# Performance work log

Measured on AMD Instinct MI355X. Metric: run time of the kernel, lower is better.

Reference implementation:

```python
import jax, jax.numpy as jnp
import numpy as np

HIDDEN = 256
NUM_STEPS = 3
N_NODES = 200000
N_GRAPHS = 512


def setup_inputs() -> dict:
    key = jax.random.key(0)
    ks = jax.random.split(key, 8)
    h = HIDDEN
    x = jax.random.normal(ks[0], (N_NODES, h), dtype=jnp.float32)
    batch = jnp.sort(jax.random.randint(ks[1], (N_NODES,), 0, N_GRAPHS)).astype(jnp.int64)
    s_ih = 1.0 / np.sqrt(2 * h)
    s_hh = 1.0 / np.sqrt(h)
    # LSTM (input 2h -> hidden h), PyTorch gate order i,f,g,o
    W_ih = jax.random.uniform(ks[2], (4 * h, 2 * h), jnp.float32, -s_ih, s_ih)
    W_hh = jax.random.uniform(ks[3], (4 * h, h), jnp.float32, -s_hh, s_hh)
    b_ih = jax.random.uniform(ks[4], (4 * h,), jnp.float32, -s_hh, s_hh)
    b_hh = jax.random.uniform(ks[5], (4 * h,), jnp.float32, -s_hh, s_hh)
    # out_proj: Linear(2h -> h)
    s_o = 1.0 / np.sqrt(2 * h)
    W_out = jax.random.uniform(ks[6], (h, 2 * h), jnp.float32, -s_o, s_o)
    b_out = jax.random.uniform(ks[7], (h,), jnp.float32, -s_o, s_o)
    return {"x": x, "batch": batch, "W_ih": W_ih, "W_hh": W_hh,
            "b_ih": b_ih, "b_hh": b_hh, "W_out": W_out, "b_out": b_out,
            "n_graphs": N_GRAPHS}


def _set2set(x, batch, W_ih, W_hh, b_ih, b_hh, n_graphs):
    h = x.shape[1]
    hs = jnp.zeros((n_graphs, h), x.dtype)
    cs = jnp.zeros((n_graphs, h), x.dtype)
    q_star = jnp.zeros((n_graphs, 2 * h), x.dtype)
    for _ in range(NUM_STEPS):
        # LSTM step (PyTorch gate order: i, f, g, o)
        gates = q_star @ W_ih.T + hs @ W_hh.T + (b_ih + b_hh)  # [B, 4h]
        i_g, f_g, g_g, o_g = jnp.split(gates, 4, axis=-1)
        cs = jax.nn.sigmoid(f_g) * cs + jax.nn.sigmoid(i_g) * jnp.tanh(g_g)
        hs = jax.nn.sigmoid(o_g) * jnp.tanh(cs)
        q = hs  # [B, h]
        # attention logits per node
        e = jnp.sum(x * q[batch], axis=-1)  # [N]
        # segment softmax over nodes of each graph
        m = jax.ops.segment_max(e, batch, num_segments=n_graphs)
        a = jnp.exp(e - m[batch])
        denom = jax.ops.segment_sum(a, batch, num_segments=n_graphs)
        a = a / denom[batch]
        # weighted readout
        r = jax.ops.segment_sum(a[:, None] * x, batch, num_segments=n_graphs)  # [B, h]
        q_star = jnp.concatenate([q, r], axis=-1)  # [B, 2h]
    return q_star


def reference(x, batch, W_ih, W_hh, b_ih, b_hh, W_out, b_out, n_graphs):
    q_star = _set2set(x, batch.astype(jnp.int32), W_ih, W_hh, b_ih, b_hh, n_graphs)
    return q_star @ W_out.T + b_out
```

## Files before the change

kernel.cpp:

```cpp
#include <hip/hip_runtime.h>
#include <hip/hip_bf16.h>

#define HID 256
#define NG 512

__device__ __forceinline__ float sigmoidf_(float v) { return 1.f / (1.f + __expf(-v)); }

__global__ __launch_bounds__(256) void prep_kernel(
    const float* __restrict__ W_ih, const float* __restrict__ W_hh,
    const float* __restrict__ b_ih, const float* __restrict__ b_hh,
    float* __restrict__ Wcat, float* __restrict__ bcat)
{
    int idx = blockIdx.x * 256 + threadIdx.x;
    if (idx < 1024 * 512) {
        int k = idx & 511;
        float v = W_ih[idx];
        if (k < 256) v += W_hh[(idx >> 9) * 256 + k];
        Wcat[idx] = v;
    }
    if (idx < 1024) bcat[idx] = b_ih[idx] + b_hh[idx];
}

__global__ __launch_bounds__(256) void find_starts(
    const int* __restrict__ batch, int n, int* __restrict__ starts)
{
    int g = blockIdx.x * 256 + threadIdx.x;
    if (g > NG) return;
    if (g == NG) { starts[NG] = n; return; }
    int lo = 0, hi = n;
    while (lo < hi) {
        int mid = (lo + hi) >> 1;
        if (batch[mid] < g) lo = mid + 1; else hi = mid;
    }
    starts[g] = lo;
}

__global__ __launch_bounds__(256) void attn_kernel(
    const float* __restrict__ x, const int* __restrict__ starts,
    const float* __restrict__ gp0, const float* __restrict__ gp1,
    const float* __restrict__ bcat, float* __restrict__ cs,
    float* __restrict__ qs, int step0)
{
    __shared__ __align__(16) float ql[HID];
    __shared__ __align__(16) float red[4][HID];
    __shared__ float mw[4], lw[4];

    const int g = blockIdx.x;
    const int tid = threadIdx.x;

    float ig, fg, gg, og, cp;
    if (step0) {
        ig = bcat[tid]; fg = bcat[256 + tid]; gg = bcat[512 + tid]; og = bcat[768 + tid];
        cp = 0.f;
    } else {
        const float* a0 = gp0 + (size_t)g * 1024;
        const float* a1 = gp1 + (size_t)g * 1024;
        ig = a0[tid]       + a1[tid]       + bcat[tid];
        fg = a0[256 + tid] + a1[256 + tid] + bcat[256 + tid];
        gg = a0[512 + tid] + a1[512 + tid] + bcat[512 + tid];
        og = a0[768 + tid] + a1[768 + tid] + bcat[768 + tid];
        cp = cs[g * HID + tid];
    }
    float cn = sigmoidf_(fg) * cp + sigmoidf_(ig) * tanhf(gg);
    float h  = sigmoidf_(og) * tanhf(cn);
    cs[g * HID + tid] = cn;
    qs[(size_t)g * 512 + tid] = h;
    ql[tid] = h;

    const int s0 = starts[g];
    const int nn = starts[g + 1] - s0;
    if (nn <= 0) { qs[(size_t)g * 512 + HID + tid] = 0.f; return; }
    __syncthreads();

    const int w = tid >> 6, lane = tid & 63;
    const int j = lane >> 3;
    const int s = lane & 7;

    float4 qf[8];
    #pragma unroll
    for (int k = 0; k < 8; ++k) qf[k] = *(const float4*)&ql[k * 32 + s * 4];

    const int nch = (nn + 7) >> 3;
    const int last = s0 + nn - 1;
    const float NEG = -3.402823466e38f;

    float m_run = NEG, l_run = 0.f;
    float4 racc[8] = {};
    float4 xc[8], xn[8];

    int c = w;
    if (c < nch) {
        int node = s0 + c * 8 + j; if (node > last) node = last;
        const float* bp = x + (size_t)node * HID + s * 4;
        #pragma unroll
        for (int k = 0; k < 8; ++k) xc[k] = *(const float4*)(bp + k * 32);
    }
    for (; c < nch; c += 4) {
        if (c + 4 < nch) {
            int node = s0 + (c + 4) * 8 + j; if (node > last) node = last;
            const float* bp = x + (size_t)node * HID + s * 4;
            #pragma unroll
            for (int k = 0; k < 8; ++k) xn[k] = *(const float4*)(bp + k * 32);
        }
        const bool valid = (c * 8 + j) < nn;

        float e = 0.f;
        #pragma unroll
        for (int k = 0; k < 8; ++k)
            e += xc[k].x * qf[k].x + xc[k].y * qf[k].y + xc[k].z * qf[k].z + xc[k].w * qf[k].w;
        e += __shfl_xor(e, 1); e += __shfl_xor(e, 2); e += __shfl_xor(e, 4);
        e = valid ? e : NEG;

        float mc = e;
        mc = fmaxf(mc, __shfl_xor(mc, 8));
        mc = fmaxf(mc, __shfl_xor(mc, 16));
        mc = fmaxf(mc, __shfl_xor(mc, 32));
        float m_new = fmaxf(m_run, mc);
        float alpha = __expf(m_run - m_new);
        float p = valid ? __expf(e - m_new) : 0.f;
        float ps = p;
        ps += __shfl_xor(ps, 8); ps += __shfl_xor(ps, 16); ps += __shfl_xor(ps, 32);
        l_run = l_run * alpha + ps;
        m_run = m_new;
        #pragma unroll
        for (int k = 0; k < 8; ++k) {
            racc[k].x = racc[k].x * alpha + p * xc[k].x;
            racc[k].y = racc[k].y * alpha + p * xc[k].y;
            racc[k].z = racc[k].z * alpha + p * xc[k].z;
            racc[k].w = racc[k].w * alpha + p * xc[k].w;
        }
        #pragma unroll
        for (int k = 0; k < 8; ++k) xc[k] = xn[k];
    }

    #pragma unroll
    for (int k = 0; k < 8; ++k) {
        racc[k].x += __shfl_xor(racc[k].x, 8);
        racc[k].y += __shfl_xor(racc[k].y, 8);
        racc[k].z += __shfl_xor(racc[k].z, 8);
        racc[k].w += __shfl_xor(racc[k].w, 8);
        racc[k].x += __shfl_xor(racc[k].x, 16);
        racc[k].y += __shfl_xor(racc[k].y, 16);
        racc[k].z += __shfl_xor(racc[k].z, 16);
        racc[k].w += __shfl_xor(racc[k].w, 16);
        racc[k].x += __shfl_xor(racc[k].x, 32);
        racc[k].y += __shfl_xor(racc[k].y, 32);
        racc[k].z += __shfl_xor(racc[k].z, 32);
        racc[k].w += __shfl_xor(racc[k].w, 32);
    }
    if (j == 0) {
        #pragma unroll
        for (int k = 0; k < 8; ++k) *(float4*)&red[w][k * 32 + s * 4] = racc[k];
        if (s == 0) { mw[w] = m_run; lw[w] = l_run; }
    }
    __syncthreads();

    float M = fmaxf(fmaxf(mw[0], mw[1]), fmaxf(mw[2], mw[3]));
    float f0 = __expf(mw[0] - M), f1 = __expf(mw[1] - M);
    float f2 = __expf(mw[2] - M), f3 = __expf(mw[3] - M);
    float L = lw[0] * f0 + lw[1] * f1 + lw[2] * f2 + lw[3] * f3;
    float r = red[0][tid] * f0 + red[1][tid] * f1 + red[2][tid] * f2 + red[3][tid] * f3;
    qs[(size_t)g * 512 + HID + tid] = r / L;
}

__global__ __launch_bounds__(256) void gemm_splitk(
    const float* __restrict__ A, int lda,
    const float* __restrict__ B, int ldb,
    float* __restrict__ Cp, int ldc, int KS, size_t slice_stride)
{
    __shared__ float As[16][76];
    __shared__ float Bs[16][76];
    const int tid = threadIdx.x;
    const int tx = tid & 15, ty = tid >> 4;
    const int m0 = blockIdx.y * 64, n0 = blockIdx.x * 64;
    const int kb = blockIdx.z * KS;
    const int r = tid >> 2, kc = (tid & 3) << 2;
    float acc[4][4] = {};

    const float* Ap = &A[(size_t)(m0 + r) * lda + kb + kc];
    const float* Bp = &B[(size_t)(n0 + r) * ldb + kb + kc];
    float4 av = *(const float4*)Ap;
    float4 bv = *(const float4*)Bp;

    for (int k0 = 0; k0 < KS; k0 += 16) {
        As[kc + 0][r] = av.x; As[kc + 1][r] = av.y; As[kc + 2][r] = av.z; As[kc + 3][r] = av.w;
        Bs[kc + 0][r] = bv.x; Bs[kc + 1][r] = bv.y; Bs[kc + 2][r] = bv.z; Bs[kc + 3][r] = bv.w;
        __syncthreads();
        if (k0 + 16 < KS) {
            av = *(const float4*)(Ap + k0 + 16);
            bv = *(const float4*)(Bp + k0 + 16);
        }
        #pragma unroll
        for (int kk = 0; kk < 16; ++kk) {
            float4 a = *(const float4*)&As[kk][ty << 2];
            float4 b = *(const float4*)&Bs[kk][tx << 2];
            acc[0][0] += a.x * b.x; acc[0][1] += a.x * b.y; acc[0][2] += a.x * b.z; acc[0][3] += a.x * b.w;
            acc[1][0] += a.y * b.x; acc[1][1] += a.y * b.y; acc[1][2] += a.y * b.z; acc[1][3] += a.y * b.w;
            acc[2][0] += a.z * b.x; acc[2][1] += a.z * b.y; acc[2][2] += a.z * b.z; acc[2][3] += a.z * b.w;
            acc[3][0] += a.w * b.x; acc[3][1] += a.w * b.y; acc[3][2] += a.w * b.z; acc[3][3] += a.w * b.w;
        }
        __syncthreads();
    }
    float* out = Cp + blockIdx.z * slice_stride;
    #pragma unroll
    for (int i = 0; i < 4; ++i) {
        float4 o = make_float4(acc[i][0], acc[i][1], acc[i][2], acc[i][3]);
        *(float4*)&out[(size_t)(m0 + ty * 4 + i) * ldc + n0 + (tx << 2)] = o;
    }
}

__global__ __launch_bounds__(256) void finalize_out(
    const float* __restrict__ op, const float* __restrict__ b_out,
    float* __restrict__ out)
{
    int i = blockIdx.x * 256 + threadIdx.x;
    if (i < 512 * 256) {
        float v = op[i] + op[131072 + i] + op[262144 + i] + op[393216 + i] + b_out[i & 255];
        out[i] = v;
    }
}

extern "C" void kernel_launch(void* const* d_in, const int* in_sizes, int n_in,
                              void* d_out, int out_size, void* d_ws, size_t ws_size,
                              hipStream_t stream)
{
    const float* x     = (const float*)d_in[0];
    const int*   batch = (const int*)d_in[1];
    const float* W_ih  = (const float*)d_in[2];
    const float* W_hh  = (const float*)d_in[3];
    const float* b_ih  = (const float*)d_in[4];
    const float* b_hh  = (const float*)d_in[5];
    const float* W_out = (const float*)d_in[6];
    const float* b_out = (const float*)d_in[7];
    float* out = (float*)d_out;
    const int n = in_sizes[1];
    (void)n_in; (void)out_size; (void)ws_size;

    char* ws = (char*)d_ws;
    float* qs      = (float*)(ws);
    float* cs      = (float*)(ws + 0x100000);
    float* gates_p = (float*)(ws + 0x180000);
    float* Wcat    = (float*)(ws + 0x580000);
    float* bcat    = (float*)(ws + 0x780000);
    int*   starts  = (int*)  (ws + 0x781000);
    float* out_p   = (float*)(ws + 0x790000);

    prep_kernel<<<2048, 256, 0, stream>>>(W_ih, W_hh, b_ih, b_hh, Wcat, bcat);
    find_starts<<<3, 256, 0, stream>>>(batch, n, starts);

    for (int step = 0; step < 3; ++step) {
        if (step > 0) {
            gemm_splitk<<<dim3(16, 8, 2), 256, 0, stream>>>(
                qs, 512, Wcat, 512, gates_p, 1024, 256, (size_t)512 * 1024);
        }
        attn_kernel<<<NG, 256, 0, stream>>>(
            x, starts, gates_p, gates_p + (size_t)512 * 1024, bcat, cs, qs, step == 0);
    }
    gemm_splitk<<<dim3(4, 8, 4), 256, 0, stream>>>(
        qs, 512, W_out, 512, out_p, 256, 128, (size_t)512 * 256);
    finalize_out<<<512, 256, 0, stream>>>(out_p, b_out, out);
}
```

Baseline: 413.5 us.

## Fuse all Set2Set stages into one cooperative persistent kernel with grid syncs

```diff
diff --git a/kernel.cpp b/kernel.cpp
--- a/kernel.cpp
+++ b/kernel.cpp
@@ -1,222 +1,244 @@
 #include <hip/hip_runtime.h>
 #include <hip/hip_bf16.h>
+#include <hip/hip_cooperative_groups.h>
+
+namespace cg = cooperative_groups;
 
 #define HID 256
 #define NG 512
+#define NBLK 256
 
 __device__ __forceinline__ float sigmoidf_(float v) { return 1.f / (1.f + __expf(-v)); }
 
-__global__ __launch_bounds__(256) void prep_kernel(
-    const float* __restrict__ W_ih, const float* __restrict__ W_hh,
-    const float* __restrict__ b_ih, const float* __restrict__ b_hh,
-    float* __restrict__ Wcat, float* __restrict__ bcat)
-{
-    int idx = blockIdx.x * 256 + threadIdx.x;
-    if (idx < 1024 * 512) {
-        int k = idx & 511;
-        float v = W_ih[idx];
-        if (k < 256) v += W_hh[(idx >> 9) * 256 + k];
-        Wcat[idx] = v;
-    }
-    if (idx < 1024) bcat[idx] = b_ih[idx] + b_hh[idx];
-}
-
-__global__ __launch_bounds__(256) void find_starts(
-    const int* __restrict__ batch, int n, int* __restrict__ starts)
-{
-    int g = blockIdx.x * 256 + threadIdx.x;
-    if (g > NG) return;
-    if (g == NG) { starts[NG] = n; return; }
-    int lo = 0, hi = n;
-    while (lo < hi) {
-        int mid = (lo + hi) >> 1;
-        if (batch[mid] < g) lo = mid + 1; else hi = mid;
-    }
-    starts[g] = lo;
-}
-
-__global__ __launch_bounds__(256) void attn_kernel(
+struct SM {
+    float As[16][76];
+    float Bs[16][76];
+    float ql[HID];
+    float red[4][HID];
+    float mw[4], lw[4];
+};
+
+__device__ __forceinline__ void gemm_tile(
+    const float* __restrict__ A, int lda, const float* __restrict__ B, int ldb,
+    float* __restrict__ C, int ldc, int m0, int n0, int kb, int KS,
+    SM& sm, int tid)
+{
+    const int tx = tid & 15, ty = tid >> 4;
+    const int r = tid >> 2, kc = (tid & 3) << 2;
+    float acc[4][4] = {};
+    const float* Ap = &A[(size_t)(m0 + r) * lda + kb + kc];
+    const float* Bp = &B[(size_t)(n0 + r) * ldb + kb + kc];
+    float4 av = *(const float4*)Ap;
+    float4 bv = *(const float4*)Bp;
+    for (int k0 = 0; k0 < KS; k0 += 16) {
+        sm.As[kc + 0][r] = av.x; sm.As[kc + 1][r] = av.y;
+        sm.As[kc + 2][r] = av.z; sm.As[kc + 3][r] = av.w;
+        sm.Bs[kc + 0][r] = bv.x; sm.Bs[kc + 1][r] = bv.y;
+        sm.Bs[kc + 2][r] = bv.z; sm.Bs[kc + 3][r] = bv.w;
+        __syncthreads();
+        if (k0 + 16 < KS) {
+            av = *(const float4*)(Ap + k0 + 16);
+            bv = *(const float4*)(Bp + k0 + 16);
+        }
+        #pragma unroll
+        for (int kk = 0; kk < 16; ++kk) {
+            float4 a  = *(const float4*)&sm.As[kk][ty << 2];
+            float4 b4 = *(const float4*)&sm.Bs[kk][tx << 2];
+            acc[0][0] += a.x * b4.x; acc[0][1] += a.x * b4.y; acc[0][2] += a.x * b4.z; acc[0][3] += a.x * b4.w;
+            acc[1][0] += a.y * b4.x; acc[1][1] += a.y * b4.y; acc[1][2] += a.y * b4.z; acc[1][3] += a.y * b4.w;
+            acc[2][0] += a.z * b4.x; acc[2][1] += a.z * b4.y; acc[2][2] += a.z * b4.z; acc[2][3] += a.z * b4.w;
+            acc[3][0] += a.w * b4.x; acc[3][1] += a.w * b4.y; acc[3][2] += a.w * b4.z; acc[3][3] += a.w * b4.w;
+        }
+        __syncthreads();
+    }
+    #pragma unroll
+    for (int i = 0; i < 4; ++i) {
+        float4 o = make_float4(acc[i][0], acc[i][1], acc[i][2], acc[i][3]);
+        *(float4*)&C[(size_t)(m0 + ty * 4 + i) * ldc + n0 + (tx << 2)] = o;
+    }
+}
+
+__device__ void attn_graph(
     const float* __restrict__ x, const int* __restrict__ starts,
-    const float* __restrict__ gp0, const float* __restrict__ gp1,
-    const float* __restrict__ bcat, float* __restrict__ cs,
-    float* __restrict__ qs, int step0)
-{
-    __shared__ __align__(16) float ql[HID];
-    __shared__ __align__(16) float red[4][HID];
-    __shared__ float mw[4], lw[4];
-
-    const int g = blockIdx.x;
-    const int tid = threadIdx.x;
-
-    float ig, fg, gg, og, cp;
+    const float* __restrict__ gp, const float* __restrict__ bcat,
+    float* __restrict__ qs, float& cstate,
+    int g, int tid, int step0, SM& sm)
+{
+    float ig, fg, gg, og;
     if (step0) {
         ig = bcat[tid]; fg = bcat[256 + tid]; gg = bcat[512 + tid]; og = bcat[768 + tid];
-        cp = 0.f;
     } else {
-        const float* a0 = gp0 + (size_t)g * 1024;
-        const float* a1 = gp1 + (size_t)g * 1024;
+        const float* a0 = gp + (size_t)g * 1024;
+        const float* a1 = a0 + (size_t)512 * 1024;
         ig = a0[tid]       + a1[tid]       + bcat[tid];
         fg = a0[256 + tid] + a1[256 + tid] + bcat[256 + tid];
         gg = a0[512 + tid] + a1[512 + tid] + bcat[512 + tid];
         og = a0[768 + tid] + a1[768 + tid] + bcat[768 + tid];
-        cp = cs[g * HID + tid];
-    }
+    }
+    float cp = step0 ? 0.f : cstate;
     float cn = sigmoidf_(fg) * cp + sigmoidf_(ig) * tanhf(gg);
     float h  = sigmoidf_(og) * tanhf(cn);
-    cs[g * HID + tid] = cn;
+    cstate = cn;
     qs[(size_t)g * 512 + tid] = h;
-    ql[tid] = h;
+    sm.ql[tid] = h;
 
     const int s0 = starts[g];
     const int nn = starts[g + 1] - s0;
-    if (nn <= 0) { qs[(size_t)g * 512 + HID + tid] = 0.f; return; }
     __syncthreads();
 
-    const int w = tid >> 6, lane = tid & 63;
-    const int j = lane >> 3;
-    const int s = lane & 7;
-
-    float4 qf[8];
-    #pragma unroll
-    for (int k = 0; k < 8; ++k) qf[k] = *(const float4*)&ql[k * 32 + s * 4];
-
-    const int nch = (nn + 7) >> 3;
-    const int last = s0 + nn - 1;
-    const float NEG = -3.402823466e38f;
-
-    float m_run = NEG, l_run = 0.f;
-    float4 racc[8] = {};
-    float4 xc[8], xn[8];
-
-    int c = w;
-    if (c < nch) {
-        int node = s0 + c * 8 + j; if (node > last) node = last;
-        const float* bp = x + (size_t)node * HID + s * 4;
+    float rout = 0.f;
+    if (nn > 0) {
+        const int w = tid >> 6, lane = tid & 63;
+        const int j = lane >> 3;
+        const int s = lane & 7;
+
+        float4 qf[8];
         #pragma unroll
-        for (int k = 0; k < 8; ++k) xc[k] = *(const float4*)(bp + k * 32);
-    }
-    for (; c < nch; c += 4) {
-        if (c + 4 < nch) {
-            int node = s0 + (c + 4) * 8 + j; if (node > last) node = last;
+        for (int k = 0; k < 8; ++k) qf[k] = *(const float4*)&sm.ql[k * 32 + s * 4];
+
+        const int nch = (nn + 7) >> 3;
+        const int last = s0 + nn - 1;
+        const float NEG = -3.402823466e38f;
+
+        float m_run = NEG, l_run = 0.f;
+        float4 racc[8] = {};
+        float4 xc[8], xn[8];
+
+        int c = w;
+        if (c < nch) {
+            int node = s0 + c * 8 + j; if (node > last) node = last;
             const float* bp = x + (size_t)node * HID + s * 4;
             #pragma unroll
-            for (int k = 0; k < 8; ++k) xn[k] = *(const float4*)(bp + k * 32);
-        }
-        const bool valid = (c * 8 + j) < nn;
-
-        float e = 0.f;
-        #pragma unroll
-        for (int k = 0; k < 8; ++k)
-            e += xc[k].x * qf[k].x + xc[k].y * qf[k].y + xc[k].z * qf[k].z + xc[k].w * qf[k].w;
-        e += __shfl_xor(e, 1); e += __shfl_xor(e, 2); e += __shfl_xor(e, 4);
-        e = valid ? e : NEG;
-
-        float mc = e;
-        mc = fmaxf(mc, __shfl_xor(mc, 8));
-        mc = fmaxf(mc, __shfl_xor(mc, 16));
-        mc = fmaxf(mc, __shfl_xor(mc, 32));
-        float m_new = fmaxf(m_run, mc);
-        float alpha = __expf(m_run - m_new);
-        float p = valid ? __expf(e - m_new) : 0.f;
-        float ps = p;
-        ps += __shfl_xor(ps, 8); ps += __shfl_xor(ps, 16); ps += __shfl_xor(ps, 32);
-        l_run = l_run * alpha + ps;
-        m_run = m_new;
+            for (int k = 0; k < 8; ++k) xc[k] = *(const float4*)(bp + k * 32);
+        }
+        for (; c < nch; c += 4) {
+            if (c + 4 < nch) {
+                int node = s0 + (c + 4) * 8 + j; if (node > last) node = last;
+                const float* bp = x + (size_t)node * HID + s * 4;
+                #pragma unroll
+                for (int k = 0; k < 8; ++k) xn[k] = *(const float4*)(bp + k * 32);
+            }
+            const bool valid = (c * 8 + j) < nn;
+
+            float e = 0.f;
+            #pragma unroll
+            for (int k = 0; k < 8; ++k)
+                e += xc[k].x * qf[k].x + xc[k].y * qf[k].y + xc[k].z * qf[k].z + xc[k].w * qf[k].w;
+            e += __shfl_xor(e, 1); e += __shfl_xor(e, 2); e += __shfl_xor(e, 4);
+            e = valid ? e : NEG;
+
+            float mc = e;
+            mc = fmaxf(mc, __shfl_xor(mc, 8));
+            mc = fmaxf(mc, __shfl_xor(mc, 16));
+            mc = fmaxf(mc, __shfl_xor(mc, 32));
+            float m_new = fmaxf(m_run, mc);
+            float alpha = __expf(m_run - m_new);
+            float p = valid ? __expf(e - m_new) : 0.f;
+            float ps = p;
+            ps += __shfl_xor(ps, 8); ps += __shfl_xor(ps, 16); ps += __shfl_xor(ps, 32);
+            l_run = l_run * alpha + ps;
+            m_run = m_new;
+            #pragma unroll
+            for (int k = 0; k < 8; ++k) {
+                racc[k].x = racc[k].x * alpha + p * xc[k].x;
+                racc[k].y = racc[k].y * alpha + p * xc[k].y;
+                racc[k].z = racc[k].z * alpha + p * xc[k].z;
+                racc[k].w = racc[k].w * alpha + p * xc[k].w;
+            }
+            #pragma unroll
+            for (int k = 0; k < 8; ++k) xc[k] = xn[k];
+        }
+
         #pragma unroll
         for (int k = 0; k < 8; ++k) {
-            racc[k].x = racc[k].x * alpha + p * xc[k].x;
-            racc[k].y = racc[k].y * alpha + p * xc[k].y;
-            racc[k].z = racc[k].z * alpha + p * xc[k].z;
-            racc[k].w = racc[k].w * alpha + p * xc[k].w;
-        }
-        #pragma unroll
-        for (int k = 0; k < 8; ++k) xc[k] = xn[k];
-    }
+            racc[k].x += __shfl_xor(racc[k].x, 8);  racc[k].y += __shfl_xor(racc[k].y, 8);
+            racc[k].z += __shfl_xor(racc[k].z, 8);  racc[k].w += __shfl_xor(racc[k].w, 8);
+            racc[k].x += __shfl_xor(racc[k].x, 16); racc[k].y += __shfl_xor(racc[k].y, 16);
+            racc[k].z += __shfl_xor(racc[k].z, 16); racc[k].w += __shfl_xor(racc[k].w, 16);
+            racc[k].x += __shfl_xor(racc[k].x, 32); racc[k].y += __shfl_xor(racc[k].y, 32);
+            racc[k].z += __shfl_xor(racc[k].z, 32); racc[k].w += __shfl_xor(racc[k].w, 32);
+        }
+        if (j == 0) {
+            #pragma unroll
+            for (int k = 0; k < 8; ++k) *(float4*)&sm.red[w][k * 32 + s * 4] = racc[k];
+            if (s == 0) { sm.mw[w] = m_run; sm.lw[w] = l_run; }
+        }
+        __syncthreads();
+
+        float M = fmaxf(fmaxf(sm.mw[0], sm.mw[1]), fmaxf(sm.mw[2], sm.mw[3]));
+        float f0 = __expf(sm.mw[0] - M), f1 = __expf(sm.mw[1] - M);
+        float f2 = __expf(sm.mw[2] - M), f3 = __expf(sm.mw[3] - M);
+        float L = sm.lw[0] * f0 + sm.lw[1] * f1 + sm.lw[2] * f2 + sm.lw[3] * f3;
+        float r = sm.red[0][tid] * f0 + sm.red[1][tid] * f1
+                + sm.red[2][tid] * f2 + sm.red[3][tid] * f3;
+        rout = r / L;
+    }
+    qs[(size_t)g * 512 + HID + tid] = rout;
+    __syncthreads();
+}
+
+__global__ __launch_bounds__(256) void fused_kernel(
+    const float* __restrict__ x, const int* __restrict__ batch,
+    const float* __restrict__ W_ih, const float* __restrict__ W_hh,
+    const float* __restrict__ b_ih, const float* __restrict__ b_hh,
+    const float* __restrict__ W_out, const float* __restrict__ b_out,
+    float* __restrict__ out, int n, char* __restrict__ ws)
+{
+    __shared__ SM sm;
+    float* qs     = (float*)(ws);
+    float* gp     = (float*)(ws + 0x100000);
+    float* Wcat   = (float*)(ws + 0x500000);
+    float* bcat   = (float*)(ws + 0x700000);
+    int*   starts = (int*)  (ws + 0x701000);
+    float* op     = (float*)(ws + 0x710000);
+
+    cg::grid_group grid = cg::this_grid();
+    const int b = blockIdx.x, tid = threadIdx.x;
+    const int gtid = b * 256 + tid;
 
     #pragma unroll
-    for (int k = 0; k < 8; ++k) {
-        racc[k].x += __shfl_xor(racc[k].x, 8);
-        racc[k].y += __shfl_xor(racc[k].y, 8);
-        racc[k].z += __shfl_xor(racc[k].z, 8);
-        racc[k].w += __shfl_xor(racc[k].w, 8);
-        racc[k].x += __shfl_xor(racc[k].x, 16);
-        racc[k].y += __shfl_xor(racc[k].y, 16);
-        racc[k].z += __shfl_xor(racc[k].z, 16);
-        racc[k].w += __shfl_xor(racc[k].w, 16);
-        racc[k].x += __shfl_xor(racc[k].x, 32);
-        racc[k].y += __shfl_xor(racc[k].y, 32);
-        racc[k].z += __shfl_xor(racc[k].z, 32);
-        racc[k].w += __shfl_xor(racc[k].w, 32);
-    }
-    if (j == 0) {
-        #pragma unroll
-        for (int k = 0; k < 8; ++k) *(float4*)&red[w][k * 32 + s * 4] = racc[k];
-        if (s == 0) { mw[w] = m_run; lw[w] = l_run; }
-    }
-    __syncthreads();
-
-    float M = fmaxf(fmaxf(mw[0], mw[1]), fmaxf(mw[2], mw[3]));
-    float f0 = __expf(mw[0] - M), f1 = __expf(mw[1] - M);
-    float f2 = __expf(mw[2] - M), f3 = __expf(mw[3] - M);
-    float L = lw[0] * f0 + lw[1] * f1 + lw[2] * f2 + lw[3] * f3;
-    float r = red[0][tid] * f0 + red[1][tid] * f1 + red[2][tid] * f2 + red[3][tid] * f3;
-    qs[(size_t)g * 512 + HID + tid] = r / L;
-}
-
-__global__ __launch_bounds__(256) void gemm_splitk(
-    const float* __restrict__ A, int lda,
-    const float* __restrict__ B, int ldb,
-    float* __restrict__ Cp, int ldc, int KS, size_t slice_stride)
-{
-    __shared__ float As[16][76];
-    __shared__ float Bs[16][76];
-    const int tid = threadIdx.x;
-    const int tx = tid & 15, ty = tid >> 4;
-    const int m0 = blockIdx.y * 64, n0 = blockIdx.x * 64;
-    const int kb = blockIdx.z * KS;
-    const int r = tid >> 2, kc = (tid & 3) << 2;
-    float acc[4][4] = {};
-
-    const float* Ap = &A[(size_t)(m0 + r) * lda + kb + kc];
-    const float* Bp = &B[(size_t)(n0 + r) * ldb + kb + kc];
-    float4 av = *(const float4*)Ap;
-    float4 bv = *(const float4*)Bp;
-
-    for (int k0 = 0; k0 < KS; k0 += 16) {
-        As[kc + 0][r] = av.x; As[kc + 1][r] = av.y; As[kc + 2][r] = av.z; As[kc + 3][r] = av.w;
-        Bs[kc + 0][r] = bv.x; Bs[kc + 1][r] = bv.y; Bs[kc + 2][r] = bv.z; Bs[kc + 3][r] = bv.w;
-        __syncthreads();
-        if (k0 + 16 < KS) {
-            av = *(const float4*)(Ap + k0 + 16);
-            bv = *(const float4*)(Bp + k0 + 16);
-        }
-        #pragma unroll
-        for (int kk = 0; kk < 16; ++kk) {
-            float4 a = *(const float4*)&As[kk][ty << 2];
-            float4 b = *(const float4*)&Bs[kk][tx << 2];
-            acc[0][0] += a.x * b.x; acc[0][1] += a.x * b.y; acc[0][2] += a.x * b.z; acc[0][3] += a.x * b.w;
-            acc[1][0] += a.y * b.x; acc[1][1] += a.y * b.y; acc[1][2] += a.y * b.z; acc[1][3] += a.y * b.w;
-            acc[2][0] += a.z * b.x; acc[2][1] += a.z * b.y; acc[2][2] += a.z * b.z; acc[2][3] += a.z * b.w;
-            acc[3][0] += a.w * b.x; acc[3][1] += a.w * b.y; acc[3][2] += a.w * b.z; acc[3][3] += a.w * b.w;
-        }
-        __syncthreads();
-    }
-    float* out = Cp + blockIdx.z * slice_stride;
-    #pragma unroll
-    for (int i = 0; i < 4; ++i) {
-        float4 o = make_float4(acc[i][0], acc[i][1], acc[i][2], acc[i][3]);
-        *(float4*)&out[(size_t)(m0 + ty * 4 + i) * ldc + n0 + (tx << 2)] = o;
-    }
-}
-
-__global__ __launch_bounds__(256) void finalize_out(
-    const float* __restrict__ op, const float* __restrict__ b_out,
-    float* __restrict__ out)
-{
-    int i = blockIdx.x * 256 + threadIdx.x;
-    if (i < 512 * 256) {
-        float v = op[i] + op[131072 + i] + op[262144 + i] + op[393216 + i] + b_out[i & 255];
-        out[i] = v;
+    for (int t = 0; t < 2; ++t) {
+        int o = (gtid * 2 + t) * 4;
+        int k = o & 511, row = o >> 9;
+        float4 v = *(const float4*)&W_ih[o];
+        if (k < 256) {
+            float4 u = *(const float4*)&W_hh[row * 256 + k];
+            v.x += u.x; v.y += u.y; v.z += u.z; v.w += u.w;
+        }
+        *(float4*)&Wcat[o] = v;
+    }
+    if (gtid < 1024) bcat[gtid] = b_ih[gtid] + b_hh[gtid];
+    for (int i = gtid; i < n; i += NBLK * 256) {
+        int b1 = batch[i];
+        int b0 = (i == 0) ? -1 : batch[i - 1];
+        for (int g2 = b0 + 1; g2 <= b1; ++g2) starts[g2] = i;
+        if (i == n - 1) for (int g2 = b1 + 1; g2 <= NG; ++g2) starts[g2] = n;
+    }
+    grid.sync();
+
+    float c0 = 0.f, c1 = 0.f;
+    for (int step = 0; step < 3; ++step) {
+        if (step > 0) {
+            int bz = b >> 7, by = (b >> 4) & 7, bx = b & 15;
+            gemm_tile(qs, 512, Wcat, 512, gp + (size_t)bz * 512 * 1024, 1024,
+                      by * 64, bx * 64, bz * 256, 256, sm, tid);
+            grid.sync();
+        }
+        attn_graph(x, starts, gp, bcat, qs, c0, 2 * b,     tid, step == 0, sm);
+        attn_graph(x, starts, gp, bcat, qs, c1, 2 * b + 1, tid, step == 0, sm);
+        grid.sync();
+    }
+
+    if (b < 128) {
+        int bz = b >> 5, by = (b >> 2) & 7, bx = b & 3;
+        gemm_tile(qs, 512, W_out, 512, op + (size_t)bz * 512 * 256, 256,
+                  by * 64, bx * 64, bz * 128, 128, sm, tid);
+    }
+    grid.sync();
+    {
+        int i0 = gtid, i1 = gtid + 65536;
+        out[i0] = op[i0] + op[131072 + i0] + op[262144 + i0] + op[393216 + i0] + b_out[i0 & 255];
+        out[i1] = op[i1] + op[131072 + i1] + op[262144 + i1] + op[393216 + i1] + b_out[i1 & 255];
     }
 }
 
@@ -233,30 +255,13 @@
     const float* W_out = (const float*)d_in[6];
     const float* b_out = (const float*)d_in[7];
     float* out = (float*)d_out;
-    const int n = in_sizes[1];
+    int n = in_sizes[1];
+    char* ws = (char*)d_ws;
     (void)n_in; (void)out_size; (void)ws_size;
 
-    char* ws = (char*)d_ws;
-    float* qs      = (float*)(ws);
-    float* cs      = (float*)(ws + 0x100000);
-    float* gates_p = (float*)(ws + 0x180000);
-    float* Wcat    = (float*)(ws + 0x580000);
-    float* bcat    = (float*)(ws + 0x780000);
-    int*   starts  = (int*)  (ws + 0x781000);
-    float* out_p   = (float*)(ws + 0x790000);
-
-    prep_kernel<<<2048, 256, 0, stream>>>(W_ih, W_hh, b_ih, b_hh, Wcat, bcat);
-    find_starts<<<3, 256, 0, stream>>>(batch, n, starts);
-
-    for (int step = 0; step < 3; ++step) {
-        if (step > 0) {
-            gemm_splitk<<<dim3(16, 8, 2), 256, 0, stream>>>(
-                qs, 512, Wcat, 512, gates_p, 1024, 256, (size_t)512 * 1024);
-        }
-        attn_kernel<<<NG, 256, 0, stream>>>(
-            x, starts, gates_p, gates_p + (size_t)512 * 1024, bcat, cs, qs, step == 0);
-    }
-    gemm_splitk<<<dim3(4, 8, 4), 256, 0, stream>>>(
-        qs, 512, W_out, 512, out_p, 256, 128, (size_t)512 * 256);
-    finalize_out<<<512, 256, 0, stream>>>(out_p, b_out, out);
-}
+    void* args[] = { (void*)&x, (void*)&batch, (void*)&W_ih, (void*)&W_hh,
+                     (void*)&b_ih, (void*)&b_hh, (void*)&W_out, (void*)&b_out,
+                     (void*)&out, (void*)&n, (void*)&ws };
+    hipLaunchCooperativeKernel((const void*)fused_kernel, dim3(NBLK), dim3(256),
+                               args, 0, stream);
+}
```

Result: slower. 627.8 us (+51.8%).

## Deepen x prefetch, keep per-lane online softmax, fuse prep and starts kernels

Applied to the files above, without the earlier changes.

```diff
diff --git a/kernel.cpp b/kernel.cpp
--- a/kernel.cpp
+++ b/kernel.cpp
@@ -9,37 +9,39 @@
 __global__ __launch_bounds__(256) void prep_kernel(
     const float* __restrict__ W_ih, const float* __restrict__ W_hh,
     const float* __restrict__ b_ih, const float* __restrict__ b_hh,
-    float* __restrict__ Wcat, float* __restrict__ bcat)
-{
-    int idx = blockIdx.x * 256 + threadIdx.x;
-    if (idx < 1024 * 512) {
-        int k = idx & 511;
-        float v = W_ih[idx];
-        if (k < 256) v += W_hh[(idx >> 9) * 256 + k];
-        Wcat[idx] = v;
-    }
-    if (idx < 1024) bcat[idx] = b_ih[idx] + b_hh[idx];
-}
-
-__global__ __launch_bounds__(256) void find_starts(
-    const int* __restrict__ batch, int n, int* __restrict__ starts)
-{
-    int g = blockIdx.x * 256 + threadIdx.x;
-    if (g > NG) return;
-    if (g == NG) { starts[NG] = n; return; }
-    int lo = 0, hi = n;
-    while (lo < hi) {
-        int mid = (lo + hi) >> 1;
-        if (batch[mid] < g) lo = mid + 1; else hi = mid;
-    }
-    starts[g] = lo;
-}
-
-__global__ __launch_bounds__(256) void attn_kernel(
+    const int* __restrict__ batch, int n,
+    float* __restrict__ Wcat, float* __restrict__ bcat, int* __restrict__ starts)
+{
+    int b = blockIdx.x, tid = threadIdx.x;
+    if (b < 512) {
+        int o = (b * 256 + tid) * 4;
+        int k = o & 511, row = o >> 9;
+        float4 v = *(const float4*)&W_ih[o];
+        if (k < 256) {
+            float4 u = *(const float4*)&W_hh[row * 256 + k];
+            v.x += u.x; v.y += u.y; v.z += u.z; v.w += u.w;
+        }
+        *(float4*)&Wcat[o] = v;
+    } else if (b < 516) {
+        int i = (b - 512) * 256 + tid;
+        bcat[i] = b_ih[i] + b_hh[i];
+    } else {
+        int g = (b - 516) * 256 + tid;
+        if (g > NG) return;
+        if (g == NG) { starts[NG] = n; return; }
+        int lo = 0, hi = n;
+        while (lo < hi) {
+            int mid = (lo + hi) >> 1;
+            if (batch[mid] < g) lo = mid + 1; else hi = mid;
+        }
+        starts[g] = lo;
+    }
+}
+
+__global__ __launch_bounds__(256, 2) void attn_kernel(
     const float* __restrict__ x, const int* __restrict__ starts,
-    const float* __restrict__ gp0, const float* __restrict__ gp1,
-    const float* __restrict__ bcat, float* __restrict__ cs,
-    float* __restrict__ qs, int step0)
+    const float* __restrict__ gp, const float* __restrict__ bcat,
+    float* __restrict__ cs, float* __restrict__ qs, int step0)
 {
     __shared__ __align__(16) float ql[HID];
     __shared__ __align__(16) float red[4][HID];
@@ -48,19 +50,18 @@
     const int g = blockIdx.x;
     const int tid = threadIdx.x;
 
-    float ig, fg, gg, og, cp;
+    float ig, fg, gg, og;
     if (step0) {
         ig = bcat[tid]; fg = bcat[256 + tid]; gg = bcat[512 + tid]; og = bcat[768 + tid];
-        cp = 0.f;
     } else {
-        const float* a0 = gp0 + (size_t)g * 1024;
-        const float* a1 = gp1 + (size_t)g * 1024;
+        const float* a0 = gp + (size_t)g * 1024;
+        const float* a1 = a0 + (size_t)512 * 1024;
         ig = a0[tid]       + a1[tid]       + bcat[tid];
         fg = a0[256 + tid] + a1[256 + tid] + bcat[256 + tid];
         gg = a0[512 + tid] + a1[512 + tid] + bcat[512 + tid];
         og = a0[768 + tid] + a1[768 + tid] + bcat[768 + tid];
-        cp = cs[g * HID + tid];
-    }
+    }
+    float cp = step0 ? 0.f : cs[g * HID + tid];
     float cn = sigmoidf_(fg) * cp + sigmoidf_(ig) * tanhf(gg);
     float h  = sigmoidf_(og) * tanhf(cn);
     cs[g * HID + tid] = cn;
@@ -86,67 +87,90 @@
 
     float m_run = NEG, l_run = 0.f;
     float4 racc[8] = {};
-    float4 xc[8], xn[8];
+    float4 xA[8], xB[8];
+
+    if (w < nch) {
+        int node = s0 + w * 8 + j; if (node > last) node = last;
+        const float* bp = x + (size_t)node * HID + s * 4;
+        #pragma unroll
+        for (int k = 0; k < 8; ++k) xA[k] = *(const float4*)(bp + k * 32);
+    }
+    if (w + 4 < nch) {
+        int node = s0 + (w + 4) * 8 + j; if (node > last) node = last;
+        const float* bp = x + (size_t)node * HID + s * 4;
+        #pragma unroll
+        for (int k = 0; k < 8; ++k) xB[k] = *(const float4*)(bp + k * 32);
+    }
+
+    #define PROCESS(XB, CC)                                                   \
+    {                                                                         \
+        const bool valid = ((CC) * 8 + j) < nn;                               \
+        float e = 0.f;                                                        \
+        _Pragma("unroll")                                                     \
+        for (int k = 0; k < 8; ++k)                                           \
+            e += XB[k].x * qf[k].x + XB[k].y * qf[k].y                        \
+               + XB[k].z * qf[k].z + XB[k].w * qf[k].w;                       \
+        e += __shfl_xor(e, 1); e += __shfl_xor(e, 2); e += __shfl_xor(e, 4);  \
+        e = valid ? e : NEG;                                                  \
+        float m_new = fmaxf(m_run, e);                                        \
+        float alpha = __expf(m_run - m_new);                                  \
+        float p = valid ? __expf(e - m_new) : 0.f;                            \
+        l_run = l_run * alpha + p;                                            \
+        m_run = m_new;                                                        \
+        _Pragma("unroll")                                                     \
+        for (int k = 0; k < 8; ++k) {                                         \
+            racc[k].x = racc[k].x * alpha + p * XB[k].x;                      \
+            racc[k].y = racc[k].y * alpha + p * XB[k].y;                      \
+            racc[k].z = racc[k].z * alpha + p * XB[k].z;                      \
+            racc[k].w = racc[k].w * alpha + p * XB[k].w;                      \
+        }                                                                     \
+    }
 
     int c = w;
-    if (c < nch) {
-        int node = s0 + c * 8 + j; if (node > last) node = last;
-        const float* bp = x + (size_t)node * HID + s * 4;
-        #pragma unroll
-        for (int k = 0; k < 8; ++k) xc[k] = *(const float4*)(bp + k * 32);
-    }
-    for (; c < nch; c += 4) {
-        if (c + 4 < nch) {
-            int node = s0 + (c + 4) * 8 + j; if (node > last) node = last;
-            const float* bp = x + (size_t)node * HID + s * 4;
+    for (; c + 4 < nch; c += 8) {
+        {
+            float4 xn[8];
+            if (c + 8 < nch) {
+                int node = s0 + (c + 8) * 8 + j; if (node > last) node = last;
+                const float* bp = x + (size_t)node * HID + s * 4;
+                #pragma unroll
+                for (int k = 0; k < 8; ++k) xn[k] = *(const float4*)(bp + k * 32);
+            }
+            PROCESS(xA, c);
             #pragma unroll
-            for (int k = 0; k < 8; ++k) xn[k] = *(const float4*)(bp + k * 32);
-        }
-        const bool valid = (c * 8 + j) < nn;
-
-        float e = 0.f;
-        #pragma unroll
-        for (int k = 0; k < 8; ++k)
-            e += xc[k].x * qf[k].x + xc[k].y * qf[k].y + xc[k].z * qf[k].z + xc[k].w * qf[k].w;
-        e += __shfl_xor(e, 1); e += __shfl_xor(e, 2); e += __shfl_xor(e, 4);
-        e = valid ? e : NEG;
-
-        float mc = e;
-        mc = fmaxf(mc, __shfl_xor(mc, 8));
-        mc = fmaxf(mc, __shfl_xor(mc, 16));
-        mc = fmaxf(mc, __shfl_xor(mc, 32));
-        float m_new = fmaxf(m_run, mc);
-        float alpha = __expf(m_run - m_new);
-        float p = valid ? __expf(e - m_new) : 0.f;
-        float ps = p;
-        ps += __shfl_xor(ps, 8); ps += __shfl_xor(ps, 16); ps += __shfl_xor(ps, 32);
-        l_run = l_run * alpha + ps;
-        m_run = m_new;
+            for (int k = 0; k < 8; ++k) xA[k] = xn[k];
+        }
+        {
+            float4 xn[8];
+            if (c + 12 < nch) {
+                int node = s0 + (c + 12) * 8 + j; if (node > last) node = last;
+                const float* bp = x + (size_t)node * HID + s * 4;
+                #pragma unroll
+                for (int k = 0; k < 8; ++k) xn[k] = *(const float4*)(bp + k * 32);
+            }
+            PROCESS(xB, c + 4);
+            #pragma unroll
+            for (int k = 0; k < 8; ++k) xB[k] = xn[k];
+        }
+    }
+    if (c < nch) PROCESS(xA, c);
+    #undef PROCESS
+
+    #pragma unroll
+    for (int bit = 8; bit <= 32; bit <<= 1) {
+        float m2 = __shfl_xor(m_run, bit);
+        float l2 = __shfl_xor(l_run, bit);
+        float M  = fmaxf(m_run, m2);
+        float a1 = __expf(m_run - M), a2 = __expf(m2 - M);
+        l_run = l_run * a1 + l2 * a2;
         #pragma unroll
         for (int k = 0; k < 8; ++k) {
-            racc[k].x = racc[k].x * alpha + p * xc[k].x;
-            racc[k].y = racc[k].y * alpha + p * xc[k].y;
-            racc[k].z = racc[k].z * alpha + p * xc[k].z;
-            racc[k].w = racc[k].w * alpha + p * xc[k].w;
-        }
-        #pragma unroll
-        for (int k = 0; k < 8; ++k) xc[k] = xn[k];
-    }
-
-    #pragma unroll
-    for (int k = 0; k < 8; ++k) {
-        racc[k].x += __shfl_xor(racc[k].x, 8);
-        racc[k].y += __shfl_xor(racc[k].y, 8);
-        racc[k].z += __shfl_xor(racc[k].z, 8);
-        racc[k].w += __shfl_xor(racc[k].w, 8);
-        racc[k].x += __shfl_xor(racc[k].x, 16);
-        racc[k].y += __shfl_xor(racc[k].y, 16);
-        racc[k].z += __shfl_xor(racc[k].z, 16);
-        racc[k].w += __shfl_xor(racc[k].w, 16);
-        racc[k].x += __shfl_xor(racc[k].x, 32);
-        racc[k].y += __shfl_xor(racc[k].y, 32);
-        racc[k].z += __shfl_xor(racc[k].z, 32);
-        racc[k].w += __shfl_xor(racc[k].w, 32);
+            racc[k].x = racc[k].x * a1 + __shfl_xor(racc[k].x, bit) * a2;
+            racc[k].y = racc[k].y * a1 + __shfl_xor(racc[k].y, bit) * a2;
+            racc[k].z = racc[k].z * a1 + __shfl_xor(racc[k].z, bit) * a2;
+            racc[k].w = racc[k].w * a1 + __shfl_xor(racc[k].w, bit) * a2;
+        }
+        m_run = M;
     }
     if (j == 0) {
         #pragma unroll
@@ -215,8 +239,7 @@
 {
     int i = blockIdx.x * 256 + threadIdx.x;
     if (i < 512 * 256) {
-        float v = op[i] + op[131072 + i] + op[262144 + i] + op[393216 + i] + b_out[i & 255];
-        out[i] = v;
+        out[i] = op[i] + op[131072 + i] + op[262144 + i] + op[393216 + i] + b_out[i & 255];
     }
 }
 
@@ -237,26 +260,24 @@
     (void)n_in; (void)out_size; (void)ws_size;
 
     char* ws = (char*)d_ws;
-    float* qs      = (float*)(ws);
-    float* cs      = (float*)(ws + 0x100000);
-    float* gates_p = (float*)(ws + 0x180000);
-    float* Wcat    = (float*)(ws + 0x580000);
-    float* bcat    = (float*)(ws + 0x780000);
-    int*   starts  = (int*)  (ws + 0x781000);
-    float* out_p   = (float*)(ws + 0x790000);
-
-    prep_kernel<<<2048, 256, 0, stream>>>(W_ih, W_hh, b_ih, b_hh, Wcat, bcat);
-    find_starts<<<3, 256, 0, stream>>>(batch, n, starts);
-
+    float* qs     = (float*)(ws);
+    float* cs     = (float*)(ws + 0x100000);
+    float* gp     = (float*)(ws + 0x180000);
+    float* Wcat   = (float*)(ws + 0x580000);
+    float* bcat   = (float*)(ws + 0x780000);
+    int*   starts = (int*)  (ws + 0x781000);
+    float* op     = (float*)(ws + 0x790000);
+
+    prep_kernel<<<519, 256, 0, stream>>>(W_ih, W_hh, b_ih, b_hh, batch, n,
+                                         Wcat, bcat, starts);
     for (int step = 0; step < 3; ++step) {
         if (step > 0) {
             gemm_splitk<<<dim3(16, 8, 2), 256, 0, stream>>>(
-                qs, 512, Wcat, 512, gates_p, 1024, 256, (size_t)512 * 1024);
-        }
-        attn_kernel<<<NG, 256, 0, stream>>>(
-            x, starts, gates_p, gates_p + (size_t)512 * 1024, bcat, cs, qs, step == 0);
+                qs, 512, Wcat, 512, gp, 1024, 256, (size_t)512 * 1024);
+        }
+        attn_kernel<<<NG, 256, 0, stream>>>(x, starts, gp, bcat, cs, qs, step == 0);
     }
     gemm_splitk<<<dim3(4, 8, 4), 256, 0, stream>>>(
-        qs, 512, W_out, 512, out_p, 256, 128, (size_t)512 * 256);
-    finalize_out<<<512, 256, 0, stream>>>(out_p, b_out, out);
-}
+        qs, 512, W_out, 512, op, 256, 128, (size_t)512 * 256);
+    finalize_out<<<512, 256, 0, stream>>>(op, b_out, out);
+}
```

After: 455.1 us. 10.1% more time.
